# Optimization experiments

Measured on AMD Instinct MI355X. Metric: run time of the kernel, lower is better.

The kernel has to match this reference:

```python
import jax, jax.numpy as jnp
import numpy as np

H, D_IN, D_Q, D_V = 8, 16, 32, 32
N = M = 4096


def setup_inputs() -> dict:
    key = jax.random.key(0)
    ks = jax.random.split(key, 12)
    s_in = 1.0 / np.sqrt(D_IN)
    s_fc = 1.0 / np.sqrt(H * D_V)
    return {
        "x": jax.random.normal(ks[0], (N, D_IN), jnp.float32),
        "y": jax.random.normal(ks[1], (M, D_IN), jnp.float32),
        # per-head stacked weights: [H, D_IN, D_Q/ D_V]
        "Wq": jax.random.uniform(ks[2], (H, D_IN, D_Q), jnp.float32, -s_in, s_in),
        "bq": jax.random.uniform(ks[3], (H, D_Q), jnp.float32, -s_in, s_in),
        "Wk": jax.random.uniform(ks[4], (H, D_IN, D_Q), jnp.float32, -s_in, s_in),
        "bk": jax.random.uniform(ks[5], (H, D_Q), jnp.float32, -s_in, s_in),
        "Wv": jax.random.uniform(ks[6], (H, D_IN, D_V), jnp.float32, -s_in, s_in),
        "bv": jax.random.uniform(ks[7], (H, D_V), jnp.float32, -s_in, s_in),
        "Wo": jax.random.uniform(ks[8], (H * D_V, D_IN), jnp.float32, -s_fc, s_fc),
        "bo": jax.random.uniform(ks[9], (D_IN,), jnp.float32, -s_fc, s_fc),
    }


def reference(x, y, Wq, bq, Wk, bk, Wv, bv, Wo, bo):
    # batched per-head projections (fuses the 8 tiny Linears of the torch loop)
    q = jnp.einsum("nd,hdq->hnq", x, Wq) + bq[:, None, :]   # [H, N, D_Q]
    k = jnp.einsum("md,hdq->hmq", y, Wk) + bk[:, None, :]   # [H, M, D_Q]
    v = jnp.einsum("md,hdv->hmv", y, Wv) + bv[:, None, :]   # [H, M, D_V]
    scores = jnp.einsum("hnq,hmq->hnm", q, k) / jnp.sqrt(jnp.float32(D_Q))
    attn = jax.nn.softmax(scores, axis=-1)                  # [H, N, M]
    heads = jnp.einsum("hnm,hmv->hnv", attn, v)             # [H, N, D_V]
    # torch.cat(head_outputs, dim=-1): head h occupies columns [h*D_V:(h+1)*D_V]
    concat = jnp.transpose(heads, (1, 0, 2)).reshape(x.shape[0], H * D_V)
    return concat @ Wo + bo                                  # [N, D_IN]
```

## Files before the change

### kernel.cpp

```cpp
#include <hip/hip_runtime.h>
#include <hip/hip_bf16.h>

typedef __attribute__((ext_vector_type(8))) short bf16x8;
typedef __attribute__((ext_vector_type(4))) float f32x4;
typedef unsigned short u16;
typedef unsigned int u32;

#define NH 8
#define NN 4096
#define MM 4096

__device__ __forceinline__ u16 f2bf(float f) {
  u32 b = __float_as_uint(f);
  b += 0x7FFFu + ((b >> 16) & 1u);
  return (u16)(b >> 16);
}

__device__ __forceinline__ u32 pack_rnu(float a, float b) {
  u32 ua = __float_as_uint(a) + 0x8000u;
  u32 ub = __float_as_uint(b) + 0x8000u;
#if __has_builtin(__builtin_amdgcn_perm)
  return __builtin_amdgcn_perm(ub, ua, 0x07060302u);
#else
  return (ua >> 16) | (ub & 0xFFFF0000u);
#endif
}

#if __has_builtin(__builtin_amdgcn_exp2f)
__device__ __forceinline__ float exp2_fast(float x) { return __builtin_amdgcn_exp2f(x); }
#else
__device__ __forceinline__ float exp2_fast(float x) { return __expf(x * 0.69314718055994531f); }
#endif

__global__ __launch_bounds__(256) void proj_qk_kernel(
    const float* __restrict__ x, const float* __restrict__ y,
    const float* __restrict__ Wq, const float* __restrict__ bq,
    const float* __restrict__ Wk, const float* __restrict__ bk,
    u16* __restrict__ qs, u16* __restrict__ ks)
{
  int idx = blockIdx.x * 256 + threadIdx.x;
  int t = idx >> 15;
  int h = (idx >> 12) & 7;
  int row = idx & 4095;
  const float* src = (t ? y : x) + row * 16;
  const float* W = (t ? Wk : Wq) + (h << 9);
  const float* b = (t ? bk : bq) + (h << 5);
  const float scale = t ? 1.0f : 0.25503635116465163f;
  float4 r4[4];
#pragma unroll
  for (int i = 0; i < 4; ++i) r4[i] = ((const float4*)src)[i];
  const float* r = (const float*)r4;
  u16* out = (t ? ks : qs) + (idx & 32767) * 32;
#pragma unroll
  for (int j = 0; j < 32; ++j) {
    float a = b[j];
#pragma unroll
    for (int i = 0; i < 16; ++i) a = fmaf(r[i], W[i * 32 + j], a);
    out[j] = f2bf(a * scale);
  }
}

__global__ __launch_bounds__(256) void proj_v_kernel(
    const float* __restrict__ y, const float* __restrict__ Wv,
    const float* __restrict__ bv, u16* __restrict__ vT)
{
  __shared__ u16 sv[256][33];
  int h = blockIdx.x >> 4;
  int kb = (blockIdx.x & 15) << 8;
  int tid = threadIdx.x;
  const float* src = y + (kb + tid) * 16;
  const float* W = Wv + (h << 9);
  const float* b = bv + (h << 5);
  float4 r4[4];
#pragma unroll
  for (int i = 0; i < 4; ++i) r4[i] = ((const float4*)src)[i];
  const float* r = (const float*)r4;
#pragma unroll
  for (int j = 0; j < 32; ++j) {
    float a = b[j];
#pragma unroll
    for (int i = 0; i < 16; ++i) a = fmaf(r[i], W[i * 32 + j], a);
    sv[tid][j] = f2bf(a);
  }
  __syncthreads();
  int dv = tid >> 3;
  int c = (tid & 7) << 5;
  u16* dst = vT + (((h << 5) + dv) << 12) + kb + c;
#pragma unroll
  for (int q = 0; q < 4; ++q) {
    uint4 w;
    w.x = (u32)sv[c + q * 8 + 0][dv] | ((u32)sv[c + q * 8 + 1][dv] << 16);
    w.y = (u32)sv[c + q * 8 + 2][dv] | ((u32)sv[c + q * 8 + 3][dv] << 16);
    w.z = (u32)sv[c + q * 8 + 4][dv] | ((u32)sv[c + q * 8 + 5][dv] << 16);
    w.w = (u32)sv[c + q * 8 + 6][dv] | ((u32)sv[c + q * 8 + 7][dv] << 16);
    *(uint4*)(dst + q * 8) = w;
  }
}

#define KST 40
#define VST 72
#define VSZ (32 * VST)

__global__ __launch_bounds__(256) void flash_kernel(
    const u16* __restrict__ qs, const u16* __restrict__ ksrc,
    const u16* __restrict__ vT, float* __restrict__ accP,
    float* __restrict__ lsumP)
{
  __shared__ u16 sK[128 * KST];
  __shared__ u16 sVT[2 * VSZ];
  const int h = blockIdx.y;
  const int qt = blockIdx.x;
  const int z = blockIdx.z;
  const int nIter = (MM / 128) / gridDim.z;
  const int kb0 = z * (MM / gridDim.z);
  const int tid = threadIdx.x;
  const int wv = tid >> 6;
  const int lane = tid & 63;
  const int d = lane & 15;
  const int g = lane >> 4;
  const int qrow = (qt << 6) + (wv << 4) + d;

  union U4 { uint4 q; bf16x8 v; };
  U4 qf;
  qf.q = *(const uint4*)(qs + (((h << 12) + qrow) << 5) + (g << 3));

  float lsum = 0.f;
  f32x4 acc0 = {0.f, 0.f, 0.f, 0.f};
  f32x4 acc1 = {0.f, 0.f, 0.f, 0.f};
  const f32x4 zero = {0.f, 0.f, 0.f, 0.f};

  const u16* gK = ksrc + (h << 17) + (kb0 << 5) + ((tid >> 1) << 5) + ((tid & 1) << 4);
  const u16* gV = vT + (((h << 5) + (tid >> 3)) << 12) + kb0 + ((tid & 7) << 4);
  u16* wK = sK + (tid >> 1) * KST + ((tid & 1) << 4);
  u16* wV = sVT + ((tid & 7) >> 2) * VSZ + (tid >> 3) * VST + ((tid & 7) & 3) * 16;

  {
    uint4 a = *(const uint4*)gK, b = *(const uint4*)(gK + 8);
    uint4 c = *(const uint4*)gV, e = *(const uint4*)(gV + 8);
    *(uint4*)wK = a; *(uint4*)(wK + 8) = b;
    *(uint4*)wV = c; *(uint4*)(wV + 8) = e;
  }
  __syncthreads();

  auto compute = [&](const u16* kb, const u16* vb) {
    U4 af;
    f32x4 s[4];
#pragma unroll
    for (int t = 0; t < 4; ++t) {
      af.q = *(const uint4*)(kb + (t * 16 + d) * KST + (g << 3));
      s[t] = __builtin_amdgcn_mfma_f32_16x16x32_bf16(af.v, qf.v, zero, 0, 0, 0);
    }
    float e[16];
#pragma unroll
    for (int t = 0; t < 4; ++t) {
      e[4 * t + 0] = exp2_fast(s[t].x);
      e[4 * t + 1] = exp2_fast(s[t].y);
      e[4 * t + 2] = exp2_fast(s[t].z);
      e[4 * t + 3] = exp2_fast(s[t].w);
    }
    float t0 = (e[0] + e[1]) + (e[2] + e[3]);
    float t1 = (e[4] + e[5]) + (e[6] + e[7]);
    float t2 = (e[8] + e[9]) + (e[10] + e[11]);
    float t3 = (e[12] + e[13]) + (e[14] + e[15]);
    lsum += (t0 + t1) + (t2 + t3);
    union { u32 w[4]; bf16x8 v; } pb0, pb1;
    pb0.w[0] = pack_rnu(e[0], e[1]);   pb0.w[1] = pack_rnu(e[2], e[3]);
    pb0.w[2] = pack_rnu(e[4], e[5]);   pb0.w[3] = pack_rnu(e[6], e[7]);
    pb1.w[0] = pack_rnu(e[8], e[9]);   pb1.w[1] = pack_rnu(e[10], e[11]);
    pb1.w[2] = pack_rnu(e[12], e[13]); pb1.w[3] = pack_rnu(e[14], e[15]);
    union { uint2 q2[2]; bf16x8 v; } vf;
    const u16* vp = vb + d * VST + (g << 2);
    vf.q2[0] = *(const uint2*)vp;        vf.q2[1] = *(const uint2*)(vp + 16);
    acc0 = __builtin_amdgcn_mfma_f32_16x16x32_bf16(vf.v, pb0.v, acc0, 0, 0, 0);
    vf.q2[0] = *(const uint2*)(vp + 32); vf.q2[1] = *(const uint2*)(vp + 48);
    acc0 = __builtin_amdgcn_mfma_f32_16x16x32_bf16(vf.v, pb1.v, acc0, 0, 0, 0);
    vp += 16 * VST;
    vf.q2[0] = *(const uint2*)vp;        vf.q2[1] = *(const uint2*)(vp + 16);
    acc1 = __builtin_amdgcn_mfma_f32_16x16x32_bf16(vf.v, pb0.v, acc1, 0, 0, 0);
    vf.q2[0] = *(const uint2*)(vp + 32); vf.q2[1] = *(const uint2*)(vp + 48);
    acc1 = __builtin_amdgcn_mfma_f32_16x16x32_bf16(vf.v, pb1.v, acc1, 0, 0, 0);
  };

#pragma unroll 1
  for (int it = 0; it < nIter; ++it) {
    uint4 a, b, c, e;
    if (it < nIter - 1) {
      gK += 4096; gV += 128;
      a = *(const uint4*)gK; b = *(const uint4*)(gK + 8);
      c = *(const uint4*)gV; e = *(const uint4*)(gV + 8);
    }
    compute(sK, sVT);
    compute(sK + 64 * KST, sVT + VSZ);
    __syncthreads();
    if (it < nIter - 1) {
      *(uint4*)wK = a; *(uint4*)(wK + 8) = b;
      *(uint4*)wV = c; *(uint4*)(wV + 8) = e;
      __syncthreads();
    }
  }

  lsum += __shfl_xor(lsum, 16);
  lsum += __shfl_xor(lsum, 32);
  if (g == 0)
    lsumP[((z * NH + h) << 12) + qrow] = lsum;
  float* cp = accP + z * (NN * 256) + (qrow << 8) + (h << 5) + (g << 2);
  *(float4*)cp        = make_float4(acc0.x, acc0.y, acc0.z, acc0.w);
  *(float4*)(cp + 16) = make_float4(acc1.x, acc1.y, acc1.z, acc1.w);
}

__global__ __launch_bounds__(256) void combine_kernel(
    const float* __restrict__ accP, const float* __restrict__ lsumP,
    float* __restrict__ concat, int S)
{
  int idx = blockIdx.x * 256 + threadIdx.x;
  int n = idx >> 8;
  int h = (idx & 255) >> 5;
  float o = 0.f, l = 0.f;
  for (int s = 0; s < S; ++s) {
    o += accP[s * (NN * 256) + idx];
    l += lsumP[((s * NH + h) << 12) + n];
  }
  concat[idx] = o / l;
}

__global__ __launch_bounds__(256) void out_gemm_kernel(
    const float* __restrict__ concat, const float* __restrict__ Wo,
    const float* __restrict__ bo, float* __restrict__ out)
{
  __shared__ float sWo[4096];
  int tid = threadIdx.x;
  for (int i = tid; i < 4096; i += 256) sWo[i] = Wo[i];
  __syncthreads();
  int idx = blockIdx.x * 256 + tid;
  int n = idx >> 4;
  int c = idx & 15;
  const float4* crow = (const float4*)(concat + (n << 8));
  float a = bo[c];
#pragma unroll 4
  for (int i4 = 0; i4 < 64; ++i4) {
    float4 cv = crow[i4];
    a = fmaf(cv.x, sWo[(i4 * 4 + 0) * 16 + c], a);
    a = fmaf(cv.y, sWo[(i4 * 4 + 1) * 16 + c], a);
    a = fmaf(cv.z, sWo[(i4 * 4 + 2) * 16 + c], a);
    a = fmaf(cv.w, sWo[(i4 * 4 + 3) * 16 + c], a);
  }
  out[idx] = a;
}

extern "C" void kernel_launch(void* const* d_in, const int* in_sizes, int n_in,
                              void* d_out, int out_size, void* d_ws, size_t ws_size,
                              hipStream_t stream) {
  const float* x  = (const float*)d_in[0];
  const float* y  = (const float*)d_in[1];
  const float* Wq = (const float*)d_in[2];
  const float* bq = (const float*)d_in[3];
  const float* Wk = (const float*)d_in[4];
  const float* bk = (const float*)d_in[5];
  const float* Wv = (const float*)d_in[6];
  const float* bv = (const float*)d_in[7];
  const float* Wo = (const float*)d_in[8];
  const float* bo = (const float*)d_in[9];
  float* out = (float*)d_out;

  u16* qs = (u16*)d_ws;
  u16* ks = qs + (NH * NN * 32);
  u16* vT = ks + (NH * MM * 32);
  float* concat = (float*)(vT + (NH * MM * 32));
  float* accP = concat;
  const int S = (ws_size >= (size_t)(6 + 16) * 1024 * 1024 + 512 * 1024) ? 4 : 1;
  float* lsumP = accP + (size_t)S * (NN * 256);

  hipLaunchKernelGGL(proj_qk_kernel, dim3(256), dim3(256), 0, stream,
                     x, y, Wq, bq, Wk, bk, qs, ks);
  hipLaunchKernelGGL(proj_v_kernel, dim3(128), dim3(256), 0, stream, y, Wv, bv, vT);
  hipLaunchKernelGGL(flash_kernel, dim3(64, NH, S), dim3(256), 0, stream,
                     qs, ks, vT, accP, lsumP);
  hipLaunchKernelGGL(combine_kernel, dim3(4096), dim3(256), 0, stream,
                     accP, lsumP, concat, S);
  hipLaunchKernelGGL(out_gemm_kernel, dim3(256), dim3(256), 0, stream, concat, Wo, bo, out);
}
```

Measured before the change: 71.22 us.

## Merge projection kernels, fuse split-K combine into output GEMM, vectorize V loads

```diff
diff --git a/kernel.cpp b/kernel.cpp
--- a/kernel.cpp
+++ b/kernel.cpp
@@ -32,68 +32,68 @@
 __device__ __forceinline__ float exp2_fast(float x) { return __expf(x * 0.69314718055994531f); }
 #endif
 
-__global__ __launch_bounds__(256) void proj_qk_kernel(
+__global__ __launch_bounds__(256) void proj_kernel(
     const float* __restrict__ x, const float* __restrict__ y,
     const float* __restrict__ Wq, const float* __restrict__ bq,
     const float* __restrict__ Wk, const float* __restrict__ bk,
-    u16* __restrict__ qs, u16* __restrict__ ks)
-{
-  int idx = blockIdx.x * 256 + threadIdx.x;
-  int t = idx >> 15;
-  int h = (idx >> 12) & 7;
-  int row = idx & 4095;
-  const float* src = (t ? y : x) + row * 16;
-  const float* W = (t ? Wk : Wq) + (h << 9);
-  const float* b = (t ? bk : bq) + (h << 5);
-  const float scale = t ? 1.0f : 0.25503635116465163f;
-  float4 r4[4];
-#pragma unroll
-  for (int i = 0; i < 4; ++i) r4[i] = ((const float4*)src)[i];
-  const float* r = (const float*)r4;
-  u16* out = (t ? ks : qs) + (idx & 32767) * 32;
-#pragma unroll
-  for (int j = 0; j < 32; ++j) {
-    float a = b[j];
-#pragma unroll
-    for (int i = 0; i < 16; ++i) a = fmaf(r[i], W[i * 32 + j], a);
-    out[j] = f2bf(a * scale);
-  }
-}
-
-__global__ __launch_bounds__(256) void proj_v_kernel(
-    const float* __restrict__ y, const float* __restrict__ Wv,
-    const float* __restrict__ bv, u16* __restrict__ vT)
+    const float* __restrict__ Wv, const float* __restrict__ bv,
+    u16* __restrict__ qs, u16* __restrict__ ks, u16* __restrict__ vT)
 {
   __shared__ u16 sv[256][33];
-  int h = blockIdx.x >> 4;
-  int kb = (blockIdx.x & 15) << 8;
-  int tid = threadIdx.x;
-  const float* src = y + (kb + tid) * 16;
-  const float* W = Wv + (h << 9);
-  const float* b = bv + (h << 5);
-  float4 r4[4];
-#pragma unroll
-  for (int i = 0; i < 4; ++i) r4[i] = ((const float4*)src)[i];
-  const float* r = (const float*)r4;
-#pragma unroll
-  for (int j = 0; j < 32; ++j) {
-    float a = b[j];
-#pragma unroll
-    for (int i = 0; i < 16; ++i) a = fmaf(r[i], W[i * 32 + j], a);
-    sv[tid][j] = f2bf(a);
-  }
-  __syncthreads();
-  int dv = tid >> 3;
-  int c = (tid & 7) << 5;
-  u16* dst = vT + (((h << 5) + dv) << 12) + kb + c;
-#pragma unroll
-  for (int q = 0; q < 4; ++q) {
-    uint4 w;
-    w.x = (u32)sv[c + q * 8 + 0][dv] | ((u32)sv[c + q * 8 + 1][dv] << 16);
-    w.y = (u32)sv[c + q * 8 + 2][dv] | ((u32)sv[c + q * 8 + 3][dv] << 16);
-    w.z = (u32)sv[c + q * 8 + 4][dv] | ((u32)sv[c + q * 8 + 5][dv] << 16);
-    w.w = (u32)sv[c + q * 8 + 6][dv] | ((u32)sv[c + q * 8 + 7][dv] << 16);
-    *(uint4*)(dst + q * 8) = w;
+  const int bid = blockIdx.x;
+  const int tid = threadIdx.x;
+  if (bid < 256) {
+    int idx = bid * 256 + tid;
+    int t = idx >> 15;
+    int h = (idx >> 12) & 7;
+    int row = idx & 4095;
+    const float* src = (t ? y : x) + row * 16;
+    const float* W = (t ? Wk : Wq) + (h << 9);
+    const float* b = (t ? bk : bq) + (h << 5);
+    const float scale = t ? 1.0f : 0.25503635116465163f;
+    float4 r4[4];
+#pragma unroll
+    for (int i = 0; i < 4; ++i) r4[i] = ((const float4*)src)[i];
+    const float* r = (const float*)r4;
+    u16* out = (t ? ks : qs) + (idx & 32767) * 32;
+#pragma unroll
+    for (int j = 0; j < 32; ++j) {
+      float a = b[j];
+#pragma unroll
+      for (int i = 0; i < 16; ++i) a = fmaf(r[i], W[i * 32 + j], a);
+      out[j] = f2bf(a * scale);
+    }
+  } else {
+    int vb = bid - 256;
+    int h = vb >> 4;
+    int kb = (vb & 15) << 8;
+    const float* src = y + (kb + tid) * 16;
+    const float* W = Wv + (h << 9);
+    const float* b = bv + (h << 5);
+    float4 r4[4];
+#pragma unroll
+    for (int i = 0; i < 4; ++i) r4[i] = ((const float4*)src)[i];
+    const float* r = (const float*)r4;
+#pragma unroll
+    for (int j = 0; j < 32; ++j) {
+      float a = b[j];
+#pragma unroll
+      for (int i = 0; i < 16; ++i) a = fmaf(r[i], W[i * 32 + j], a);
+      sv[tid][j] = f2bf(a);
+    }
+    __syncthreads();
+    int dv = tid >> 3;
+    int c = (tid & 7) << 5;
+    u16* dst = vT + (((h << 5) + dv) << 12) + kb + c;
+#pragma unroll
+    for (int q = 0; q < 4; ++q) {
+      uint4 w;
+      w.x = (u32)sv[c + 4 * q + 0][dv]      | ((u32)sv[c + 4 * q + 1][dv] << 16);
+      w.y = (u32)sv[c + 4 * q + 2][dv]      | ((u32)sv[c + 4 * q + 3][dv] << 16);
+      w.z = (u32)sv[c + 16 + 4 * q + 0][dv] | ((u32)sv[c + 16 + 4 * q + 1][dv] << 16);
+      w.w = (u32)sv[c + 16 + 4 * q + 2][dv] | ((u32)sv[c + 16 + 4 * q + 3][dv] << 16);
+      *(uint4*)(dst + q * 8) = w;
+    }
   }
 }
 
@@ -168,16 +168,16 @@
     pb0.w[2] = pack_rnu(e[4], e[5]);   pb0.w[3] = pack_rnu(e[6], e[7]);
     pb1.w[0] = pack_rnu(e[8], e[9]);   pb1.w[1] = pack_rnu(e[10], e[11]);
     pb1.w[2] = pack_rnu(e[12], e[13]); pb1.w[3] = pack_rnu(e[14], e[15]);
-    union { uint2 q2[2]; bf16x8 v; } vf;
-    const u16* vp = vb + d * VST + (g << 2);
-    vf.q2[0] = *(const uint2*)vp;        vf.q2[1] = *(const uint2*)(vp + 16);
+    U4 vf;
+    const u16* vp = vb + d * VST;
+    vf.q = *(const uint4*)(vp + (g << 3));
     acc0 = __builtin_amdgcn_mfma_f32_16x16x32_bf16(vf.v, pb0.v, acc0, 0, 0, 0);
-    vf.q2[0] = *(const uint2*)(vp + 32); vf.q2[1] = *(const uint2*)(vp + 48);
+    vf.q = *(const uint4*)(vp + 32 + (g << 3));
     acc0 = __builtin_amdgcn_mfma_f32_16x16x32_bf16(vf.v, pb1.v, acc0, 0, 0, 0);
     vp += 16 * VST;
-    vf.q2[0] = *(const uint2*)vp;        vf.q2[1] = *(const uint2*)(vp + 16);
+    vf.q = *(const uint4*)(vp + (g << 3));
     acc1 = __builtin_amdgcn_mfma_f32_16x16x32_bf16(vf.v, pb0.v, acc1, 0, 0, 0);
-    vf.q2[0] = *(const uint2*)(vp + 32); vf.q2[1] = *(const uint2*)(vp + 48);
+    vf.q = *(const uint4*)(vp + 32 + (g << 3));
     acc1 = __builtin_amdgcn_mfma_f32_16x16x32_bf16(vf.v, pb1.v, acc1, 0, 0, 0);
   };
 
@@ -208,43 +208,48 @@
   *(float4*)(cp + 16) = make_float4(acc1.x, acc1.y, acc1.z, acc1.w);
 }
 
-__global__ __launch_bounds__(256) void combine_kernel(
+__global__ __launch_bounds__(256) void out_gemm_kernel(
     const float* __restrict__ accP, const float* __restrict__ lsumP,
-    float* __restrict__ concat, int S)
-{
-  int idx = blockIdx.x * 256 + threadIdx.x;
-  int n = idx >> 8;
-  int h = (idx & 255) >> 5;
-  float o = 0.f, l = 0.f;
-  for (int s = 0; s < S; ++s) {
-    o += accP[s * (NN * 256) + idx];
-    l += lsumP[((s * NH + h) << 12) + n];
-  }
-  concat[idx] = o / l;
-}
-
-__global__ __launch_bounds__(256) void out_gemm_kernel(
-    const float* __restrict__ concat, const float* __restrict__ Wo,
-    const float* __restrict__ bo, float* __restrict__ out)
+    const float* __restrict__ Wo, const float* __restrict__ bo,
+    float* __restrict__ out, int S)
 {
   __shared__ float sWo[4096];
-  int tid = threadIdx.x;
+  __shared__ float sC[16][260];
+  __shared__ float sD[16][8];
+  const int tid = threadIdx.x;
+  const int n0 = blockIdx.x << 4;
+
+  if (tid < 128) {
+    int row = tid >> 3, hh = tid & 7;
+    float l = 0.f;
+    for (int s = 0; s < S; ++s) l += lsumP[((s * NH + hh) << 12) + n0 + row];
+    sD[row][hh] = 1.0f / l;
+  }
   for (int i = tid; i < 4096; i += 256) sWo[i] = Wo[i];
   __syncthreads();
-  int idx = blockIdx.x * 256 + tid;
-  int n = idx >> 4;
-  int c = idx & 15;
-  const float4* crow = (const float4*)(concat + (n << 8));
+
+#pragma unroll
+  for (int e = 0; e < 16; ++e) {
+    float o = 0.f;
+    int gidx = ((n0 + e) << 8) + tid;
+    for (int s = 0; s < S; ++s) o += accP[s * (NN * 256) + gidx];
+    sC[e][tid] = o * sD[e][tid >> 5];
+  }
+  __syncthreads();
+
+  const int r = tid >> 4;
+  const int c = tid & 15;
+  const float* crow = &sC[r][0];
   float a = bo[c];
 #pragma unroll 4
   for (int i4 = 0; i4 < 64; ++i4) {
-    float4 cv = crow[i4];
+    float4 cv = *(const float4*)(crow + i4 * 4);
     a = fmaf(cv.x, sWo[(i4 * 4 + 0) * 16 + c], a);
     a = fmaf(cv.y, sWo[(i4 * 4 + 1) * 16 + c], a);
     a = fmaf(cv.z, sWo[(i4 * 4 + 2) * 16 + c], a);
     a = fmaf(cv.w, sWo[(i4 * 4 + 3) * 16 + c], a);
   }
-  out[idx] = a;
+  out[(n0 << 4) + tid] = a;
 }
 
 extern "C" void kernel_launch(void* const* d_in, const int* in_sizes, int n_in,
@@ -265,17 +270,14 @@
   u16* qs = (u16*)d_ws;
   u16* ks = qs + (NH * NN * 32);
   u16* vT = ks + (NH * MM * 32);
-  float* concat = (float*)(vT + (NH * MM * 32));
-  float* accP = concat;
+  float* accP = (float*)(vT + (NH * MM * 32));
   const int S = (ws_size >= (size_t)(6 + 16) * 1024 * 1024 + 512 * 1024) ? 4 : 1;
   float* lsumP = accP + (size_t)S * (NN * 256);
 
-  hipLaunchKernelGGL(proj_qk_kernel, dim3(256), dim3(256), 0, stream,
-                     x, y, Wq, bq, Wk, bk, qs, ks);
-  hipLaunchKernelGGL(proj_v_kernel, dim3(128), dim3(256), 0, stream, y, Wv, bv, vT);
+  hipLaunchKernelGGL(proj_kernel, dim3(384), dim3(256), 0, stream,
+                     x, y, Wq, bq, Wk, bk, Wv, bv, qs, ks, vT);
   hipLaunchKernelGGL(flash_kernel, dim3(64, NH, S), dim3(256), 0, stream,
                      qs, ks, vT, accP, lsumP);
-  hipLaunchKernelGGL(combine_kernel, dim3(4096), dim3(256), 0, stream,
-                     accP, lsumP, concat, S);
-  hipLaunchKernelGGL(out_gemm_kernel, dim3(256), dim3(256), 0, stream, concat, Wo, bo, out);
-}
+  hipLaunchKernelGGL(out_gemm_kernel, dim3(256), dim3(256), 0, stream,
+                     accP, lsumP, Wo, bo, out, S);
+}
```

New measurement: 73.27 us. 2.9% more time.

## Process two query tiles per wave in flash kernel and merge projection kernels

Applied to the files above, without the earlier changes.

```diff
diff --git a/kernel.cpp b/kernel.cpp
--- a/kernel.cpp
+++ b/kernel.cpp
@@ -32,68 +32,68 @@
 __device__ __forceinline__ float exp2_fast(float x) { return __expf(x * 0.69314718055994531f); }
 #endif
 
-__global__ __launch_bounds__(256) void proj_qk_kernel(
+__global__ __launch_bounds__(256) void proj_kernel(
     const float* __restrict__ x, const float* __restrict__ y,
     const float* __restrict__ Wq, const float* __restrict__ bq,
     const float* __restrict__ Wk, const float* __restrict__ bk,
-    u16* __restrict__ qs, u16* __restrict__ ks)
-{
-  int idx = blockIdx.x * 256 + threadIdx.x;
-  int t = idx >> 15;
-  int h = (idx >> 12) & 7;
-  int row = idx & 4095;
-  const float* src = (t ? y : x) + row * 16;
-  const float* W = (t ? Wk : Wq) + (h << 9);
-  const float* b = (t ? bk : bq) + (h << 5);
-  const float scale = t ? 1.0f : 0.25503635116465163f;
-  float4 r4[4];
-#pragma unroll
-  for (int i = 0; i < 4; ++i) r4[i] = ((const float4*)src)[i];
-  const float* r = (const float*)r4;
-  u16* out = (t ? ks : qs) + (idx & 32767) * 32;
-#pragma unroll
-  for (int j = 0; j < 32; ++j) {
-    float a = b[j];
-#pragma unroll
-    for (int i = 0; i < 16; ++i) a = fmaf(r[i], W[i * 32 + j], a);
-    out[j] = f2bf(a * scale);
-  }
-}
-
-__global__ __launch_bounds__(256) void proj_v_kernel(
-    const float* __restrict__ y, const float* __restrict__ Wv,
-    const float* __restrict__ bv, u16* __restrict__ vT)
+    const float* __restrict__ Wv, const float* __restrict__ bv,
+    u16* __restrict__ qs, u16* __restrict__ ks, u16* __restrict__ vT)
 {
   __shared__ u16 sv[256][33];
-  int h = blockIdx.x >> 4;
-  int kb = (blockIdx.x & 15) << 8;
-  int tid = threadIdx.x;
-  const float* src = y + (kb + tid) * 16;
-  const float* W = Wv + (h << 9);
-  const float* b = bv + (h << 5);
-  float4 r4[4];
-#pragma unroll
-  for (int i = 0; i < 4; ++i) r4[i] = ((const float4*)src)[i];
-  const float* r = (const float*)r4;
-#pragma unroll
-  for (int j = 0; j < 32; ++j) {
-    float a = b[j];
-#pragma unroll
-    for (int i = 0; i < 16; ++i) a = fmaf(r[i], W[i * 32 + j], a);
-    sv[tid][j] = f2bf(a);
-  }
-  __syncthreads();
-  int dv = tid >> 3;
-  int c = (tid & 7) << 5;
-  u16* dst = vT + (((h << 5) + dv) << 12) + kb + c;
-#pragma unroll
-  for (int q = 0; q < 4; ++q) {
-    uint4 w;
-    w.x = (u32)sv[c + q * 8 + 0][dv] | ((u32)sv[c + q * 8 + 1][dv] << 16);
-    w.y = (u32)sv[c + q * 8 + 2][dv] | ((u32)sv[c + q * 8 + 3][dv] << 16);
-    w.z = (u32)sv[c + q * 8 + 4][dv] | ((u32)sv[c + q * 8 + 5][dv] << 16);
-    w.w = (u32)sv[c + q * 8 + 6][dv] | ((u32)sv[c + q * 8 + 7][dv] << 16);
-    *(uint4*)(dst + q * 8) = w;
+  const int bid = blockIdx.x;
+  const int tid = threadIdx.x;
+  if (bid < 256) {
+    int idx = bid * 256 + tid;
+    int t = idx >> 15;
+    int h = (idx >> 12) & 7;
+    int row = idx & 4095;
+    const float* src = (t ? y : x) + row * 16;
+    const float* W = (t ? Wk : Wq) + (h << 9);
+    const float* b = (t ? bk : bq) + (h << 5);
+    const float scale = t ? 1.0f : 0.25503635116465163f;
+    float4 r4[4];
+#pragma unroll
+    for (int i = 0; i < 4; ++i) r4[i] = ((const float4*)src)[i];
+    const float* r = (const float*)r4;
+    u16* out = (t ? ks : qs) + (idx & 32767) * 32;
+#pragma unroll
+    for (int j = 0; j < 32; ++j) {
+      float a = b[j];
+#pragma unroll
+      for (int i = 0; i < 16; ++i) a = fmaf(r[i], W[i * 32 + j], a);
+      out[j] = f2bf(a * scale);
+    }
+  } else {
+    int vb = bid - 256;
+    int h = vb >> 4;
+    int kb = (vb & 15) << 8;
+    const float* src = y + (kb + tid) * 16;
+    const float* W = Wv + (h << 9);
+    const float* b = bv + (h << 5);
+    float4 r4[4];
+#pragma unroll
+    for (int i = 0; i < 4; ++i) r4[i] = ((const float4*)src)[i];
+    const float* r = (const float*)r4;
+#pragma unroll
+    for (int j = 0; j < 32; ++j) {
+      float a = b[j];
+#pragma unroll
+      for (int i = 0; i < 16; ++i) a = fmaf(r[i], W[i * 32 + j], a);
+      sv[tid][j] = f2bf(a);
+    }
+    __syncthreads();
+    int dv = tid >> 3;
+    int c = (tid & 7) << 5;
+    u16* dst = vT + (((h << 5) + dv) << 12) + kb + c;
+#pragma unroll
+    for (int q = 0; q < 4; ++q) {
+      uint4 w;
+      w.x = (u32)sv[c + 4 * q + 0][dv]      | ((u32)sv[c + 4 * q + 1][dv] << 16);
+      w.y = (u32)sv[c + 4 * q + 2][dv]      | ((u32)sv[c + 4 * q + 3][dv] << 16);
+      w.z = (u32)sv[c + 16 + 4 * q + 0][dv] | ((u32)sv[c + 16 + 4 * q + 1][dv] << 16);
+      w.w = (u32)sv[c + 16 + 4 * q + 2][dv] | ((u32)sv[c + 16 + 4 * q + 3][dv] << 16);
+      *(uint4*)(dst + q * 8) = w;
+    }
   }
 }
 
@@ -118,15 +118,17 @@
   const int lane = tid & 63;
   const int d = lane & 15;
   const int g = lane >> 4;
-  const int qrow = (qt << 6) + (wv << 4) + d;
+  const int qrowA = (qt << 7) + (wv << 5) + d;
+  const int qrowB = qrowA + 16;
 
   union U4 { uint4 q; bf16x8 v; };
-  U4 qf;
-  qf.q = *(const uint4*)(qs + (((h << 12) + qrow) << 5) + (g << 3));
-
-  float lsum = 0.f;
-  f32x4 acc0 = {0.f, 0.f, 0.f, 0.f};
-  f32x4 acc1 = {0.f, 0.f, 0.f, 0.f};
+  U4 qfA, qfB;
+  qfA.q = *(const uint4*)(qs + (((h << 12) + qrowA) << 5) + (g << 3));
+  qfB.q = *(const uint4*)(qs + (((h << 12) + qrowB) << 5) + (g << 3));
+
+  float lsA = 0.f, lsB = 0.f;
+  f32x4 accA0 = {0.f, 0.f, 0.f, 0.f}, accA1 = {0.f, 0.f, 0.f, 0.f};
+  f32x4 accB0 = {0.f, 0.f, 0.f, 0.f}, accB1 = {0.f, 0.f, 0.f, 0.f};
   const f32x4 zero = {0.f, 0.f, 0.f, 0.f};
 
   const u16* gK = ksrc + (h << 17) + (kb0 << 5) + ((tid >> 1) << 5) + ((tid & 1) << 4);
@@ -143,42 +145,63 @@
   __syncthreads();
 
   auto compute = [&](const u16* kb, const u16* vb) {
-    U4 af;
-    f32x4 s[4];
-#pragma unroll
-    for (int t = 0; t < 4; ++t) {
-      af.q = *(const uint4*)(kb + (t * 16 + d) * KST + (g << 3));
-      s[t] = __builtin_amdgcn_mfma_f32_16x16x32_bf16(af.v, qf.v, zero, 0, 0, 0);
-    }
-    float e[16];
-#pragma unroll
-    for (int t = 0; t < 4; ++t) {
-      e[4 * t + 0] = exp2_fast(s[t].x);
-      e[4 * t + 1] = exp2_fast(s[t].y);
-      e[4 * t + 2] = exp2_fast(s[t].z);
-      e[4 * t + 3] = exp2_fast(s[t].w);
-    }
-    float t0 = (e[0] + e[1]) + (e[2] + e[3]);
-    float t1 = (e[4] + e[5]) + (e[6] + e[7]);
-    float t2 = (e[8] + e[9]) + (e[10] + e[11]);
-    float t3 = (e[12] + e[13]) + (e[14] + e[15]);
-    lsum += (t0 + t1) + (t2 + t3);
-    union { u32 w[4]; bf16x8 v; } pb0, pb1;
-    pb0.w[0] = pack_rnu(e[0], e[1]);   pb0.w[1] = pack_rnu(e[2], e[3]);
-    pb0.w[2] = pack_rnu(e[4], e[5]);   pb0.w[3] = pack_rnu(e[6], e[7]);
-    pb1.w[0] = pack_rnu(e[8], e[9]);   pb1.w[1] = pack_rnu(e[10], e[11]);
-    pb1.w[2] = pack_rnu(e[12], e[13]); pb1.w[3] = pack_rnu(e[14], e[15]);
-    union { uint2 q2[2]; bf16x8 v; } vf;
-    const u16* vp = vb + d * VST + (g << 2);
-    vf.q2[0] = *(const uint2*)vp;        vf.q2[1] = *(const uint2*)(vp + 16);
-    acc0 = __builtin_amdgcn_mfma_f32_16x16x32_bf16(vf.v, pb0.v, acc0, 0, 0, 0);
-    vf.q2[0] = *(const uint2*)(vp + 32); vf.q2[1] = *(const uint2*)(vp + 48);
-    acc0 = __builtin_amdgcn_mfma_f32_16x16x32_bf16(vf.v, pb1.v, acc0, 0, 0, 0);
+    U4 kf[4];
+#pragma unroll
+    for (int t = 0; t < 4; ++t)
+      kf[t].q = *(const uint4*)(kb + (t * 16 + d) * KST + (g << 3));
+
+    union { u32 w[4]; bf16x8 v; } pbA0, pbA1, pbB0, pbB1;
+    {
+      f32x4 s0, s1, s2, s3;
+      s0 = __builtin_amdgcn_mfma_f32_16x16x32_bf16(kf[0].v, qfA.v, zero, 0, 0, 0);
+      s1 = __builtin_amdgcn_mfma_f32_16x16x32_bf16(kf[1].v, qfA.v, zero, 0, 0, 0);
+      s2 = __builtin_amdgcn_mfma_f32_16x16x32_bf16(kf[2].v, qfA.v, zero, 0, 0, 0);
+      s3 = __builtin_amdgcn_mfma_f32_16x16x32_bf16(kf[3].v, qfA.v, zero, 0, 0, 0);
+      float e[16];
+      e[0]=exp2_fast(s0.x); e[1]=exp2_fast(s0.y); e[2]=exp2_fast(s0.z); e[3]=exp2_fast(s0.w);
+      e[4]=exp2_fast(s1.x); e[5]=exp2_fast(s1.y); e[6]=exp2_fast(s1.z); e[7]=exp2_fast(s1.w);
+      e[8]=exp2_fast(s2.x); e[9]=exp2_fast(s2.y); e[10]=exp2_fast(s2.z); e[11]=exp2_fast(s2.w);
+      e[12]=exp2_fast(s3.x); e[13]=exp2_fast(s3.y); e[14]=exp2_fast(s3.z); e[15]=exp2_fast(s3.w);
+      lsA += ((e[0]+e[1])+(e[2]+e[3])) + ((e[4]+e[5])+(e[6]+e[7]))
+           + ((e[8]+e[9])+(e[10]+e[11])) + ((e[12]+e[13])+(e[14]+e[15]));
+      pbA0.w[0] = pack_rnu(e[0], e[1]);   pbA0.w[1] = pack_rnu(e[2], e[3]);
+      pbA0.w[2] = pack_rnu(e[4], e[5]);   pbA0.w[3] = pack_rnu(e[6], e[7]);
+      pbA1.w[0] = pack_rnu(e[8], e[9]);   pbA1.w[1] = pack_rnu(e[10], e[11]);
+      pbA1.w[2] = pack_rnu(e[12], e[13]); pbA1.w[3] = pack_rnu(e[14], e[15]);
+    }
+    {
+      f32x4 s0, s1, s2, s3;
+      s0 = __builtin_amdgcn_mfma_f32_16x16x32_bf16(kf[0].v, qfB.v, zero, 0, 0, 0);
+      s1 = __builtin_amdgcn_mfma_f32_16x16x32_bf16(kf[1].v, qfB.v, zero, 0, 0, 0);
+      s2 = __builtin_amdgcn_mfma_f32_16x16x32_bf16(kf[2].v, qfB.v, zero, 0, 0, 0);
+      s3 = __builtin_amdgcn_mfma_f32_16x16x32_bf16(kf[3].v, qfB.v, zero, 0, 0, 0);
+      float e[16];
+      e[0]=exp2_fast(s0.x); e[1]=exp2_fast(s0.y); e[2]=exp2_fast(s0.z); e[3]=exp2_fast(s0.w);
+      e[4]=exp2_fast(s1.x); e[5]=exp2_fast(s1.y); e[6]=exp2_fast(s1.z); e[7]=exp2_fast(s1.w);
+      e[8]=exp2_fast(s2.x); e[9]=exp2_fast(s2.y); e[10]=exp2_fast(s2.z); e[11]=exp2_fast(s2.w);
+      e[12]=exp2_fast(s3.x); e[13]=exp2_fast(s3.y); e[14]=exp2_fast(s3.z); e[15]=exp2_fast(s3.w);
+      lsB += ((e[0]+e[1])+(e[2]+e[3])) + ((e[4]+e[5])+(e[6]+e[7]))
+           + ((e[8]+e[9])+(e[10]+e[11])) + ((e[12]+e[13])+(e[14]+e[15]));
+      pbB0.w[0] = pack_rnu(e[0], e[1]);   pbB0.w[1] = pack_rnu(e[2], e[3]);
+      pbB0.w[2] = pack_rnu(e[4], e[5]);   pbB0.w[3] = pack_rnu(e[6], e[7]);
+      pbB1.w[0] = pack_rnu(e[8], e[9]);   pbB1.w[1] = pack_rnu(e[10], e[11]);
+      pbB1.w[2] = pack_rnu(e[12], e[13]); pbB1.w[3] = pack_rnu(e[14], e[15]);
+    }
+    U4 vf0, vf1, vf2, vf3;
+    const u16* vp = vb + d * VST;
+    vf0.q = *(const uint4*)(vp + (g << 3));
+    vf1.q = *(const uint4*)(vp + 32 + (g << 3));
     vp += 16 * VST;
-    vf.q2[0] = *(const uint2*)vp;        vf.q2[1] = *(const uint2*)(vp + 16);
-    acc1 = __builtin_amdgcn_mfma_f32_16x16x32_bf16(vf.v, pb0.v, acc1, 0, 0, 0);
-    vf.q2[0] = *(const uint2*)(vp + 32); vf.q2[1] = *(const uint2*)(vp + 48);
-    acc1 = __builtin_amdgcn_mfma_f32_16x16x32_bf16(vf.v, pb1.v, acc1, 0, 0, 0);
+    vf2.q = *(const uint4*)(vp + (g << 3));
+    vf3.q = *(const uint4*)(vp + 32 + (g << 3));
+    accA0 = __builtin_amdgcn_mfma_f32_16x16x32_bf16(vf0.v, pbA0.v, accA0, 0, 0, 0);
+    accA0 = __builtin_amdgcn_mfma_f32_16x16x32_bf16(vf1.v, pbA1.v, accA0, 0, 0, 0);
+    accA1 = __builtin_amdgcn_mfma_f32_16x16x32_bf16(vf2.v, pbA0.v, accA1, 0, 0, 0);
+    accA1 = __builtin_amdgcn_mfma_f32_16x16x32_bf16(vf3.v, pbA1.v, accA1, 0, 0, 0);
+    accB0 = __builtin_amdgcn_mfma_f32_16x16x32_bf16(vf0.v, pbB0.v, accB0, 0, 0, 0);
+    accB0 = __builtin_amdgcn_mfma_f32_16x16x32_bf16(vf1.v, pbB1.v, accB0, 0, 0, 0);
+    accB1 = __builtin_amdgcn_mfma_f32_16x16x32_bf16(vf2.v, pbB0.v, accB1, 0, 0, 0);
+    accB1 = __builtin_amdgcn_mfma_f32_16x16x32_bf16(vf3.v, pbB1.v, accB1, 0, 0, 0);
   };
 
 #pragma unroll 1
@@ -199,13 +222,20 @@
     }
   }
 
-  lsum += __shfl_xor(lsum, 16);
-  lsum += __shfl_xor(lsum, 32);
-  if (g == 0)
-    lsumP[((z * NH + h) << 12) + qrow] = lsum;
-  float* cp = accP + z * (NN * 256) + (qrow << 8) + (h << 5) + (g << 2);
-  *(float4*)cp        = make_float4(acc0.x, acc0.y, acc0.z, acc0.w);
-  *(float4*)(cp + 16) = make_float4(acc1.x, acc1.y, acc1.z, acc1.w);
+  lsA += __shfl_xor(lsA, 16);
+  lsA += __shfl_xor(lsA, 32);
+  lsB += __shfl_xor(lsB, 16);
+  lsB += __shfl_xor(lsB, 32);
+  if (g == 0) {
+    lsumP[((z * NH + h) << 12) + qrowA] = lsA;
+    lsumP[((z * NH + h) << 12) + qrowB] = lsB;
+  }
+  float* cpA = accP + z * (NN * 256) + (qrowA << 8) + (h << 5) + (g << 2);
+  *(float4*)cpA        = make_float4(accA0.x, accA0.y, accA0.z, accA0.w);
+  *(float4*)(cpA + 16) = make_float4(accA1.x, accA1.y, accA1.z, accA1.w);
+  float* cpB = accP + z * (NN * 256) + (qrowB << 8) + (h << 5) + (g << 2);
+  *(float4*)cpB        = make_float4(accB0.x, accB0.y, accB0.z, accB0.w);
+  *(float4*)(cpB + 16) = make_float4(accB1.x, accB1.y, accB1.z, accB1.w);
 }
 
 __global__ __launch_bounds__(256) void combine_kernel(
@@ -270,10 +300,9 @@
   const int S = (ws_size >= (size_t)(6 + 16) * 1024 * 1024 + 512 * 1024) ? 4 : 1;
   float* lsumP = accP + (size_t)S * (NN * 256);
 
-  hipLaunchKernelGGL(proj_qk_kernel, dim3(256), dim3(256), 0, stream,
-                     x, y, Wq, bq, Wk, bk, qs, ks);
-  hipLaunchKernelGGL(proj_v_kernel, dim3(128), dim3(256), 0, stream, y, Wv, bv, vT);
-  hipLaunchKernelGGL(flash_kernel, dim3(64, NH, S), dim3(256), 0, stream,
+  hipLaunchKernelGGL(proj_kernel, dim3(384), dim3(256), 0, stream,
+                     x, y, Wq, bq, Wk, bk, Wv, bv, qs, ks, vT);
+  hipLaunchKernelGGL(flash_kernel, dim3(32, NH, S), dim3(256), 0, stream,
                      qs, ks, vT, accP, lsumP);
   hipLaunchKernelGGL(combine_kernel, dim3(4096), dim3(256), 0, stream,
                      accP, lsumP, concat, S);
```

Measured after the change: 61.88 us. 1.15x faster.
